# Optimization experiments

Hardware: AMD Instinct MI355X
Metric: run time of the kernel (lower is better)

## Reference

```python
import jax, jax.numpy as jnp
import numpy as np

B, F, D, H = 16384, 10, 512, 8
DH = D // H
EPS = 1e-5


def setup_inputs() -> dict:
    key = jax.random.key(0)
    ks = jax.random.split(key, 12)
    s = 1.0 / np.sqrt(D)
    inp = {
        "x": jax.random.normal(ks[0], (B, F), dtype=jnp.float32),
        # per-feature Linear(1, D): weight (F, D), bias (F, D)
        "Wf": jax.random.normal(ks[1], (F, D), dtype=jnp.float32) * 1.0,
        "bf": jax.random.normal(ks[2], (F, D), dtype=jnp.float32) * 0.1,
        # MHA in/out projections (torch layout: out_features x in_features)
        "Wq": jax.random.normal(ks[3], (D, D), dtype=jnp.float32) * s,
        "Wk": jax.random.normal(ks[4], (D, D), dtype=jnp.float32) * s,
        "Wv": jax.random.normal(ks[5], (D, D), dtype=jnp.float32) * s,
        "bq": jax.random.normal(ks[6], (D,), dtype=jnp.float32) * 0.02,
        "bk": jax.random.normal(ks[7], (D,), dtype=jnp.float32) * 0.02,
        "bv": jax.random.normal(ks[8], (D,), dtype=jnp.float32) * 0.02,
        "Wo": jax.random.normal(ks[9], (D, D), dtype=jnp.float32) * s,
        "bo": jax.random.normal(ks[10], (D,), dtype=jnp.float32) * 0.02,
        "gamma": jnp.ones((D,), dtype=jnp.float32),
        "beta": jnp.zeros((D,), dtype=jnp.float32),
    }
    return inp


def reference(x, Wf, bf, Wq, Wk, Wv, bq, bk, bv, Wo, bo, gamma, beta):
    # Fused per-feature scalar Linear + ReLU: (B,F,1)*(F,D) + (F,D) -> (B,F,D)
    p = jax.nn.relu(x[:, :, None] * Wf[None] + bf[None])
    # Multi-head self-attention (q = k = v = p), torch Linear: y = x @ W.T + b
    def heads(t):  # (B,F,D) -> (B,H,F,DH)
        return t.reshape(B, F, H, DH).transpose(0, 2, 1, 3)
    q = heads(p @ Wq.T + bq)
    k = heads(p @ Wk.T + bk)
    v = heads(p @ Wv.T + bv)
    scores = jnp.einsum("bhqd,bhkd->bhqk", q, k) / jnp.sqrt(jnp.float32(DH))
    attn = jax.nn.softmax(scores, axis=-1)
    o = jnp.einsum("bhqk,bhkd->bhqd", attn, v)
    o = o.transpose(0, 2, 1, 3).reshape(B, F, D) @ Wo.T + bo
    # LayerNorm over last dim
    mu = jnp.mean(o, axis=-1, keepdims=True)
    var = jnp.mean(jnp.square(o - mu), axis=-1, keepdims=True)
    ln = (o - mu) * jax.lax.rsqrt(var + EPS) * gamma + beta
    # sum pool over the function/sequence axis
    return jnp.sum(ln, axis=1)  # (B, D)
```

## Files before the change

### kernel.cpp

```cpp
#include <hip/hip_runtime.h>
#include <stdint.h>


typedef __bf16 bf16;
typedef __bf16 bf16x8 __attribute__((ext_vector_type(8)));
typedef float f32x4 __attribute__((ext_vector_type(4)));

#define EPS 1e-5f

static constexpr size_t O_ELEMS   = (size_t)16384 * 10 * 512;
static constexpr size_t O_BYTES   = O_ELEMS * 2;
static constexpr size_t WQKV_ELEMS = (size_t)8 * 192 * 512;
static constexpr size_t WQKV_BYTES = WQKV_ELEMS * 2;

__device__ __forceinline__ void async_copy16(void* lds, const void* g) {
  __builtin_amdgcn_global_load_lds(
      (const __attribute__((address_space(1))) uint32_t*)g,
      (__attribute__((address_space(3))) uint32_t*)lds, 16, 0, 0);
}

__global__ __launch_bounds__(256) void pack_weights(
    const float* __restrict__ Wq, const float* __restrict__ Wk,
    const float* __restrict__ Wv, const float* __restrict__ Wo,
    bf16* __restrict__ wqkv, bf16* __restrict__ wob) {
  int idx = blockIdx.x * 256 + threadIdx.x;
#pragma unroll
  for (int u = 0; u < 4; ++u) {
    int i = idx + u * 262144;
    if (i < 786432) {
      int pr = i >> 9, k = i & 511;
      int h = pr / 192, w = pr - h * 192;
      int t = w >> 6, r = w & 63;
      const float* src = (t == 0) ? Wq : ((t == 1) ? Wk : Wv);
      wqkv[i] = (bf16)src[(h * 64 + r) * 512 + k];
    } else {
      int j = i - 786432;
      wob[j] = (bf16)Wo[j];
    }
  }
}

__global__ __launch_bounds__(256, 2) void kern_attn(
    const float* __restrict__ x, const float* __restrict__ Wf,
    const float* __restrict__ bfv, const bf16* __restrict__ wqkv,
    const float* __restrict__ bq, const float* __restrict__ bk,
    const float* __restrict__ bv, bf16* __restrict__ O) {
  __shared__ __align__(16) char sA[8 * 48 * 128];
  __shared__ __align__(16) char sU[24576];
  bf16* qkv = (bf16*)sU;
  float* sc = (float*)(sU + 19200);

  const int tid = threadIdx.x;
  const int wave = tid >> 6;
  const int lane = tid & 63;
  const int lm = lane & 15;
  const int lg = lane >> 4;
  const int b0 = blockIdx.x * 4;

#pragma unroll
  for (int it = 0; it < 12; ++it) {
    int c = tid + it * 256;
    int s = c / 384, rem = c - s * 384;
    int r = rem >> 3, kcp = rem & 7;
    int kc = kcp ^ (r & 7);
    int k = s * 64 + kc * 8;
    bf16x8 pv;
    if (r < 40) {
      int bl = r / 10, f = r - bl * 10;
      float xv = x[(b0 + bl) * 10 + f];
      const float* wf = Wf + f * 512 + k;
      const float* bp = bfv + f * 512 + k;
#pragma unroll
      for (int j = 0; j < 8; ++j) {
        float p = fmaxf(xv * wf[j] + bp[j], 0.f);
        pv[j] = (bf16)p;
      }
    } else {
#pragma unroll
      for (int j = 0; j < 8; ++j) pv[j] = (bf16)0.f;
    }
    *(bf16x8*)(sA + s * 6144 + r * 128 + kcp * 16) = pv;
  }

  const int lr = lane >> 3;
  const int kcp2 = lane & 7;
  const int kcg = kcp2 ^ lr;

  for (int h = 0; h < 8; ++h) {
    f32x4 acc[3][3];
#pragma unroll
    for (int i = 0; i < 3; ++i)
#pragma unroll
      for (int j = 0; j < 3; ++j) { f32x4 z = {0.f, 0.f, 0.f, 0.f}; acc[i][j] = z; }

    const bf16* wh = wqkv + (size_t)h * 192 * 512;

    for (int s = 0; s < 8; ++s) {
#pragma unroll
      for (int jb = 0; jb < 6; ++jb) {
        int rb = wave + 4 * jb;
        int rr = rb * 8 + lr;
        async_copy16(sU + rb * 1024, wh + (size_t)rr * 512 + s * 64 + kcg * 8);
      }
      __syncthreads();
#pragma unroll
      for (int kk = 0; kk < 2; ++kk) {
        int kcl = kk * 4 + lg;
        bf16x8 af[3], bfr[3];
#pragma unroll
        for (int mt = 0; mt < 3; ++mt) {
          int m = mt * 16 + lm;
          af[mt] = *(const bf16x8*)(sA + s * 6144 + m * 128 + ((kcl ^ (m & 7)) << 4));
        }
#pragma unroll
        for (int nt = 0; nt < 3; ++nt) {
          int n = wave * 48 + nt * 16 + lm;
          bfr[nt] = *(const bf16x8*)(sU + n * 128 + ((kcl ^ (n & 7)) << 4));
        }
#pragma unroll
        for (int mt = 0; mt < 3; ++mt)
#pragma unroll
          for (int nt = 0; nt < 3; ++nt)
            acc[mt][nt] = __builtin_amdgcn_mfma_f32_16x16x32_bf16(af[mt], bfr[nt], acc[mt][nt], 0, 0, 0);
      }
      __syncthreads();
    }

#pragma unroll
    for (int nt = 0; nt < 3; ++nt) {
      int col = wave * 48 + nt * 16 + lm;
      float bias;
      if (col < 64) bias = bq[h * 64 + col];
      else if (col < 128) bias = bk[h * 64 + col - 64];
      else bias = bv[h * 64 + col - 128];
#pragma unroll
      for (int mt = 0; mt < 3; ++mt)
#pragma unroll
        for (int r = 0; r < 4; ++r) {
          int row = mt * 16 + lg * 4 + r;
          if (row < 40) qkv[row * 200 + col] = (bf16)(acc[mt][nt][r] + bias);
        }
    }
    __syncthreads();

    {
      int b = wave;
#pragma unroll
      for (int pp = 0; pp < 2; ++pp) {
        int p = lane + pp * 64;
        if (p < 100) {
          int i = p / 10, j = p - i * 10;
          const bf16x8* qr = (const bf16x8*)(qkv + (b * 10 + i) * 200);
          const bf16x8* kr = (const bf16x8*)(qkv + (b * 10 + j) * 200 + 64);
          float d = 0.f;
#pragma unroll
          for (int c8 = 0; c8 < 8; ++c8) {
            bf16x8 qv = qr[c8], kv = kr[c8];
#pragma unroll
            for (int e = 0; e < 8; ++e) d += (float)qv[e] * (float)kv[e];
          }
          sc[(b * 10 + i) * 12 + j] = d * 0.125f;
        }
      }
    }
    __syncthreads();

    if (tid < 40) {
      float* row = sc + tid * 12;
      float m = row[0];
#pragma unroll
      for (int j = 1; j < 10; ++j) m = fmaxf(m, row[j]);
      float e[10], sum = 0.f;
#pragma unroll
      for (int j = 0; j < 10; ++j) { e[j] = __expf(row[j] - m); sum += e[j]; }
      float inv = 1.f / sum;
#pragma unroll
      for (int j = 0; j < 10; ++j) row[j] = e[j] * inv;
    }
    __syncthreads();

#pragma unroll
    for (int u = 0; u < 10; ++u) {
      int id = tid + u * 256;
      int b = id / 640, rem2 = id - b * 640;
      int i = rem2 >> 6, d = rem2 & 63;
      const float* ar = sc + (b * 10 + i) * 12;
      float o = 0.f;
#pragma unroll
      for (int j = 0; j < 10; ++j)
        o += ar[j] * (float)qkv[(b * 10 + j) * 200 + 128 + d];
      O[((size_t)(b0 + b) * 10 + i) * 512 + h * 64 + d] = (bf16)o;
    }
    __syncthreads();
  }
}

__global__ __launch_bounds__(256, 2) void kern_out(
    const bf16* __restrict__ O, const bf16* __restrict__ wob,
    const float* __restrict__ bo, const float* __restrict__ gamma,
    const float* __restrict__ beta, float* __restrict__ out) {
  __shared__ __align__(16) char sAB[71680];
  __shared__ float partial[48][4][2];
  __shared__ float stats[48][2];
  char* As = sAB;
  char* Bs = sAB + 6144;
  bf16* lnb = (bf16*)sAB;

  const int tid = threadIdx.x;
  const int wave = tid >> 6, lane = tid & 63;
  const int lm = lane & 15, lg = lane >> 4;
  const int m0 = blockIdx.x * 40;

  f32x4 acc[3][8];
#pragma unroll
  for (int i = 0; i < 3; ++i)
#pragma unroll
    for (int j = 0; j < 8; ++j) { f32x4 z = {0.f, 0.f, 0.f, 0.f}; acc[i][j] = z; }

  const int lr = lane >> 3;
  const int kcp2 = lane & 7;
  const int kcg = kcp2 ^ lr;

  for (int s = 0; s < 8; ++s) {
    {
      int rr = wave * 8 + lr;
      int rm = min(rr, 39);
      async_copy16(As + wave * 1024, O + (size_t)(m0 + rm) * 512 + s * 64 + kcg * 8);
      if (wave < 2) {
        int rr2 = (4 + wave) * 8 + lr;
        int rm2 = min(rr2, 39);
        async_copy16(As + (4 + wave) * 1024, O + (size_t)(m0 + rm2) * 512 + s * 64 + kcg * 8);
      }
    }
#pragma unroll
    for (int jb = 0; jb < 16; ++jb) {
      int rb = wave + 4 * jb;
      int n = rb * 8 + lr;
      async_copy16(Bs + rb * 1024, wob + (size_t)n * 512 + s * 64 + kcg * 8);
    }
    __syncthreads();
#pragma unroll
    for (int kk = 0; kk < 2; ++kk) {
      int kcl = kk * 4 + lg;
      bf16x8 af[3], bfr[8];
#pragma unroll
      for (int mt = 0; mt < 3; ++mt) {
        int m = mt * 16 + lm;
        af[mt] = *(const bf16x8*)(As + m * 128 + ((kcl ^ (m & 7)) << 4));
      }
#pragma unroll
      for (int nt = 0; nt < 8; ++nt) {
        int n = wave * 128 + nt * 16 + lm;
        bfr[nt] = *(const bf16x8*)(Bs + n * 128 + ((kcl ^ (n & 7)) << 4));
      }
#pragma unroll
      for (int mt = 0; mt < 3; ++mt)
#pragma unroll
        for (int nt = 0; nt < 8; ++nt)
          acc[mt][nt] = __builtin_amdgcn_mfma_f32_16x16x32_bf16(af[mt], bfr[nt], acc[mt][nt], 0, 0, 0);
    }
    __syncthreads();
  }

#pragma unroll
  for (int nt = 0; nt < 8; ++nt) {
    int col = wave * 128 + nt * 16 + lm;
    float bb = bo[col];
#pragma unroll
    for (int mt = 0; mt < 3; ++mt)
#pragma unroll
      for (int r = 0; r < 4; ++r) acc[mt][nt][r] += bb;
  }

#pragma unroll
  for (int mt = 0; mt < 3; ++mt)
#pragma unroll
    for (int r = 0; r < 4; ++r) {
      float s1 = 0.f, s2 = 0.f;
#pragma unroll
      for (int nt = 0; nt < 8; ++nt) { float v = acc[mt][nt][r]; s1 += v; s2 += v * v; }
#pragma unroll
      for (int off = 1; off < 16; off <<= 1) {
        s1 += __shfl_xor(s1, off);
        s2 += __shfl_xor(s2, off);
      }
      if (lm == 0) {
        int row = mt * 16 + lg * 4 + r;
        partial[row][wave][0] = s1;
        partial[row][wave][1] = s2;
      }
    }
  __syncthreads();
  if (tid < 48) {
    float s1 = partial[tid][0][0] + partial[tid][1][0] + partial[tid][2][0] + partial[tid][3][0];
    float s2 = partial[tid][0][1] + partial[tid][1][1] + partial[tid][2][1] + partial[tid][3][1];
    float mu = s1 * (1.f / 512.f);
    float var = s2 * (1.f / 512.f) - mu * mu;
    stats[tid][0] = mu;
    stats[tid][1] = rsqrtf(var + EPS);
  }
  __syncthreads();
#pragma unroll
  for (int mt = 0; mt < 3; ++mt)
#pragma unroll
    for (int r = 0; r < 4; ++r) {
      int row = mt * 16 + lg * 4 + r;
      float mu = stats[row][0], rr = stats[row][1];
#pragma unroll
      for (int nt = 0; nt < 8; ++nt) {
        int col = wave * 128 + nt * 16 + lm;
        lnb[row * 520 + col] = (bf16)((acc[mt][nt][r] - mu) * rr);
      }
    }
  __syncthreads();
#pragma unroll
  for (int u = 0; u < 8; ++u) {
    int id = tid + u * 256;
    int b = id >> 9, n = id & 511;
    float ssum = 0.f;
#pragma unroll
    for (int f = 0; f < 10; ++f) ssum += (float)lnb[(b * 10 + f) * 520 + n];
    out[(size_t)(blockIdx.x * 4 + b) * 512 + n] = gamma[n] * ssum + 10.f * beta[n];
  }
}

extern "C" void kernel_launch(void* const* d_in, const int* in_sizes, int n_in,
                              void* d_out, int out_size, void* d_ws, size_t ws_size,
                              hipStream_t stream) {
  const float* x     = (const float*)d_in[0];
  const float* Wf    = (const float*)d_in[1];
  const float* bfv   = (const float*)d_in[2];
  const float* Wq    = (const float*)d_in[3];
  const float* Wk    = (const float*)d_in[4];
  const float* Wv    = (const float*)d_in[5];
  const float* bq    = (const float*)d_in[6];
  const float* bk    = (const float*)d_in[7];
  const float* bv    = (const float*)d_in[8];
  const float* Wo    = (const float*)d_in[9];
  const float* bo    = (const float*)d_in[10];
  const float* gamma = (const float*)d_in[11];
  const float* beta  = (const float*)d_in[12];
  float* out = (float*)d_out;

  char* ws = (char*)d_ws;
  bf16* O    = (bf16*)ws;
  bf16* wqkv = (bf16*)(ws + O_BYTES);
  bf16* wob  = (bf16*)(ws + O_BYTES + WQKV_BYTES);

  pack_weights<<<1024, 256, 0, stream>>>(Wq, Wk, Wv, Wo, wqkv, wob);
  kern_attn<<<4096, 256, 0, stream>>>(x, Wf, bfv, wqkv, bq, bk, bv, O);
  kern_out<<<4096, 256, 0, stream>>>(O, wob, bo, gamma, beta, out);
}
```

Baseline: 842.1 us.

## Double-buffer QKV weight tiles, double batch per block, MFMA for attention scores

The attention kernel now processes 8 batch rows per block with 512 threads arranged as a 2x4 wave grid, so each 80-row activation tile has no zero padding and every weight tile loaded into LDS is reused across twice as many rows. Weight tiles are double-buffered with async global-to-LDS copies of the next k-step issued before computing the current one, which removes one barrier per step and hides load latency. QK^T scores are computed with an MFMA per wave, and softmax uses wave shuffles instead of a separate scalar pass and extra barriers. LDS use rises to roughly 150 KB per block, which may limit occupancy to one block per CU. Lanes past the 10 valid key rows in the score MFMA read Q/K rows from the neighbouring batch, and those values are masked out.

```diff
diff --git a/kernel.cpp b/kernel.cpp
--- a/kernel.cpp
+++ b/kernel.cpp
@@ -40,51 +40,56 @@
   }
 }
 
-__global__ __launch_bounds__(256, 2) void kern_attn(
+__global__ __launch_bounds__(512, 2) void kern_attn(
     const float* __restrict__ x, const float* __restrict__ Wf,
     const float* __restrict__ bfv, const bf16* __restrict__ wqkv,
     const float* __restrict__ bq, const float* __restrict__ bk,
     const float* __restrict__ bv, bf16* __restrict__ O) {
-  __shared__ __align__(16) char sA[8 * 48 * 128];
-  __shared__ __align__(16) char sU[24576];
-  bf16* qkv = (bf16*)sU;
-  float* sc = (float*)(sU + 19200);
+  __shared__ __align__(16) char sA[8 * 80 * 128];
+  __shared__ __align__(16) char sB0[24576];
+  __shared__ __align__(16) char sB1[24576];
+  __shared__ __align__(16) char sQK[88 * 256];
+
+  bf16* vbuf = (bf16*)sB1;
+  float* scp = (float*)(sB1 + 10240);
 
   const int tid = threadIdx.x;
   const int wave = tid >> 6;
   const int lane = tid & 63;
   const int lm = lane & 15;
   const int lg = lane >> 4;
-  const int b0 = blockIdx.x * 4;
-
-#pragma unroll
-  for (int it = 0; it < 12; ++it) {
-    int c = tid + it * 256;
-    int s = c / 384, rem = c - s * 384;
+  const int wm = wave >> 2;
+  const int wn = wave & 3;
+  const int b0 = blockIdx.x * 8;
+  const int lr = lane >> 3;
+  const int kcp2 = lane & 7;
+  const int kcg = kcp2 ^ lr;
+
+#pragma unroll
+  for (int jb = 0; jb < 3; ++jb) {
+    int rb = wave + 8 * jb;
+    async_copy16(sB0 + rb * 1024, wqkv + (size_t)(rb * 8 + lr) * 512 + kcg * 8);
+  }
+
+#pragma unroll
+  for (int it = 0; it < 10; ++it) {
+    int c = tid + it * 512;
+    int s = c / 640, rem = c - s * 640;
     int r = rem >> 3, kcp = rem & 7;
     int kc = kcp ^ (r & 7);
     int k = s * 64 + kc * 8;
+    int bl = r / 10, f = r - bl * 10;
+    float xv = x[(b0 + bl) * 10 + f];
+    const float* wf = Wf + f * 512 + k;
+    const float* bp = bfv + f * 512 + k;
     bf16x8 pv;
-    if (r < 40) {
-      int bl = r / 10, f = r - bl * 10;
-      float xv = x[(b0 + bl) * 10 + f];
-      const float* wf = Wf + f * 512 + k;
-      const float* bp = bfv + f * 512 + k;
-#pragma unroll
-      for (int j = 0; j < 8; ++j) {
-        float p = fmaxf(xv * wf[j] + bp[j], 0.f);
-        pv[j] = (bf16)p;
-      }
-    } else {
-#pragma unroll
-      for (int j = 0; j < 8; ++j) pv[j] = (bf16)0.f;
-    }
-    *(bf16x8*)(sA + s * 6144 + r * 128 + kcp * 16) = pv;
-  }
-
-  const int lr = lane >> 3;
-  const int kcp2 = lane & 7;
-  const int kcg = kcp2 ^ lr;
+#pragma unroll
+    for (int j = 0; j < 8; ++j) pv[j] = (bf16)fmaxf(xv * wf[j] + bp[j], 0.f);
+    *(bf16x8*)(sA + s * 10240 + r * 128 + kcp * 16) = pv;
+  }
+  __syncthreads();
+
+  const int x7 = lm & 7;
 
   for (int h = 0; h < 8; ++h) {
     f32x4 acc[3][3];
@@ -93,29 +98,34 @@
 #pragma unroll
       for (int j = 0; j < 3; ++j) { f32x4 z = {0.f, 0.f, 0.f, 0.f}; acc[i][j] = z; }
 
-    const bf16* wh = wqkv + (size_t)h * 192 * 512;
-
     for (int s = 0; s < 8; ++s) {
-#pragma unroll
-      for (int jb = 0; jb < 6; ++jb) {
-        int rb = wave + 4 * jb;
-        int rr = rb * 8 + lr;
-        async_copy16(sU + rb * 1024, wh + (size_t)rr * 512 + s * 64 + kcg * 8);
-      }
-      __syncthreads();
+      int t = h * 8 + s;
+      char* bufC = (s & 1) ? sB1 : sB0;
+      char* bufN = (s & 1) ? sB0 : sB1;
+      if (t != 63) {
+        int tn = t + 1;
+        int h2 = tn >> 3, s2 = tn & 7;
+        const bf16* srcb = wqkv + (size_t)h2 * 98304 + s2 * 64 + kcg * 8;
+#pragma unroll
+        for (int jb = 0; jb < 3; ++jb) {
+          int rb = wave + 8 * jb;
+          async_copy16(bufN + rb * 1024, srcb + (size_t)(rb * 8 + lr) * 512);
+        }
+      }
 #pragma unroll
       for (int kk = 0; kk < 2; ++kk) {
         int kcl = kk * 4 + lg;
+        int ch = (kcl ^ x7) << 4;
         bf16x8 af[3], bfr[3];
 #pragma unroll
         for (int mt = 0; mt < 3; ++mt) {
-          int m = mt * 16 + lm;
-          af[mt] = *(const bf16x8*)(sA + s * 6144 + m * 128 + ((kcl ^ (m & 7)) << 4));
+          int m = wm * 48 + mt * 16 + lm;
+          af[mt] = *(const bf16x8*)(sA + s * 10240 + m * 128 + ch);
         }
 #pragma unroll
         for (int nt = 0; nt < 3; ++nt) {
-          int n = wave * 48 + nt * 16 + lm;
-          bfr[nt] = *(const bf16x8*)(sU + n * 128 + ((kcl ^ (n & 7)) << 4));
+          int n = wn * 48 + nt * 16 + lm;
+          bfr[nt] = *(const bf16x8*)(bufC + n * 128 + ch);
         }
 #pragma unroll
         for (int mt = 0; mt < 3; ++mt)
@@ -126,70 +136,80 @@
       __syncthreads();
     }
 
-#pragma unroll
-    for (int nt = 0; nt < 3; ++nt) {
-      int col = wave * 48 + nt * 16 + lm;
-      float bias;
-      if (col < 64) bias = bq[h * 64 + col];
-      else if (col < 128) bias = bk[h * 64 + col - 64];
-      else bias = bv[h * 64 + col - 128];
-#pragma unroll
-      for (int mt = 0; mt < 3; ++mt)
-#pragma unroll
-        for (int r = 0; r < 4; ++r) {
-          int row = mt * 16 + lg * 4 + r;
-          if (row < 40) qkv[row * 200 + col] = (bf16)(acc[mt][nt][r] + bias);
+    {
+      float bias[3];
+#pragma unroll
+      for (int nt = 0; nt < 3; ++nt) {
+        int col = wn * 48 + nt * 16 + lm;
+        bias[nt] = (col < 64) ? bq[h * 64 + col]
+                 : (col < 128) ? bk[h * 64 + col - 64]
+                 : bv[h * 64 + col - 128];
+      }
+#pragma unroll
+      for (int mt = 0; mt < 3; ++mt) {
+        int rowb = wm * 48 + mt * 16 + lg * 4;
+        if (rowb < 80) {
+#pragma unroll
+          for (int r = 0; r < 4; ++r) {
+            int rw = rowb + r;
+#pragma unroll
+            for (int nt = 0; nt < 3; ++nt) {
+              int col = wn * 48 + nt * 16 + lm;
+              float val = acc[mt][nt][r] + bias[nt];
+              if (col < 128)
+                *(bf16*)(sQK + rw * 256 + (((col >> 3) ^ (rw & 7)) << 4) + (col & 7) * 2) = (bf16)val;
+              else
+                vbuf[rw * 64 + (col - 128)] = (bf16)val;
+            }
+          }
         }
+      }
     }
     __syncthreads();
 
     {
-      int b = wave;
-#pragma unroll
-      for (int pp = 0; pp < 2; ++pp) {
-        int p = lane + pp * 64;
-        if (p < 100) {
-          int i = p / 10, j = p - i * 10;
-          const bf16x8* qr = (const bf16x8*)(qkv + (b * 10 + i) * 200);
-          const bf16x8* kr = (const bf16x8*)(qkv + (b * 10 + j) * 200 + 64);
-          float d = 0.f;
-#pragma unroll
-          for (int c8 = 0; c8 < 8; ++c8) {
-            bf16x8 qv = qr[c8], kv = kr[c8];
-#pragma unroll
-            for (int e = 0; e < 8; ++e) d += (float)qv[e] * (float)kv[e];
-          }
-          sc[(b * 10 + i) * 12 + j] = d * 0.125f;
-        }
-      }
-    }
-    __syncthreads();
-
-    if (tid < 40) {
-      float* row = sc + tid * 12;
-      float m = row[0];
-#pragma unroll
-      for (int j = 1; j < 10; ++j) m = fmaxf(m, row[j]);
-      float e[10], sum = 0.f;
-#pragma unroll
-      for (int j = 0; j < 10; ++j) { e[j] = __expf(row[j] - m); sum += e[j]; }
-      float inv = 1.f / sum;
-#pragma unroll
-      for (int j = 0; j < 10; ++j) row[j] = e[j] * inv;
-    }
-    __syncthreads();
-
-#pragma unroll
-    for (int u = 0; u < 10; ++u) {
-      int id = tid + u * 256;
-      int b = id / 640, rem2 = id - b * 640;
-      int i = rem2 >> 6, d = rem2 & 63;
-      const float* ar = sc + (b * 10 + i) * 12;
-      float o = 0.f;
-#pragma unroll
-      for (int j = 0; j < 10; ++j)
-        o += ar[j] * (float)qkv[(b * 10 + j) * 200 + 128 + d];
-      O[((size_t)(b0 + b) * 10 + i) * 512 + h * 64 + d] = (bf16)o;
+      const int b = wave;
+      f32x4 sv = {0.f, 0.f, 0.f, 0.f};
+      const int rowa = b * 10 + lm;
+      const int x7r = rowa & 7;
+#pragma unroll
+      for (int kk = 0; kk < 2; ++kk) {
+        bf16x8 qf = *(const bf16x8*)(sQK + rowa * 256 + (((kk * 4 + lg) ^ x7r) << 4));
+        bf16x8 kf = *(const bf16x8*)(sQK + rowa * 256 + (((8 + kk * 4 + lg) ^ x7r) << 4));
+        sv = __builtin_amdgcn_mfma_f32_16x16x32_bf16(qf, kf, sv, 0, 0, 0);
+      }
+#pragma unroll
+      for (int r = 0; r < 4; ++r) {
+        float val = (lm < 10) ? sv[r] * 0.125f : -1e30f;
+        float mx = val;
+#pragma unroll
+        for (int off = 1; off < 16; off <<= 1) mx = fmaxf(mx, __shfl_xor(mx, off));
+        float e = __expf(val - mx);
+        float ssum = e;
+#pragma unroll
+        for (int off = 1; off < 16; off <<= 1) ssum += __shfl_xor(ssum, off);
+        int i = lg * 4 + r;
+        if (i < 10 && lm < 12) scp[(b * 10 + i) * 12 + lm] = e / ssum;
+      }
+    }
+
+    {
+      const int b = wave;
+      const int d = lane;
+      float vv[10];
+#pragma unroll
+      for (int j = 0; j < 10; ++j) vv[j] = (float)vbuf[(b * 10 + j) * 64 + d];
+      bf16* Ob = O + ((size_t)(b0 + b) * 10) * 512 + h * 64 + d;
+#pragma unroll
+      for (int i = 0; i < 10; ++i) {
+        const float* ar = scp + (b * 10 + i) * 12;
+        f32x4 a0 = *(const f32x4*)ar;
+        f32x4 a1 = *(const f32x4*)(ar + 4);
+        float o = a0[0] * vv[0] + a0[1] * vv[1] + a0[2] * vv[2] + a0[3] * vv[3]
+                + a1[0] * vv[4] + a1[1] * vv[5] + a1[2] * vv[6] + a1[3] * vv[7]
+                + ar[8] * vv[8] + ar[9] * vv[9];
+        Ob[(size_t)i * 512] = (bf16)o;
+      }
     }
     __syncthreads();
   }
@@ -348,6 +368,6 @@
   bf16* wob  = (bf16*)(ws + O_BYTES + WQKV_BYTES);
 
   pack_weights<<<1024, 256, 0, stream>>>(Wq, Wk, Wv, Wo, wqkv, wob);
-  kern_attn<<<4096, 256, 0, stream>>>(x, Wf, bfv, wqkv, bq, bk, bv, O);
+  kern_attn<<<2048, 512, 0, stream>>>(x, Wf, bfv, wqkv, bq, bk, bv, O);
   kern_out<<<4096, 256, 0, stream>>>(O, wob, bo, gamma, beta, out);
 }
```

Result: faster. 790.4 us (-6.1%).
